# Kernel optimization log

Hardware: AMD Instinct MI355X
Metric: run time of the kernel (lower is better)

Reference implementation:

```python
import jax, jax.numpy as jnp
import numpy as np
from jax import lax

B, C, H, W = 8, 256, 128, 128
RED = 16


def _disk(r):
    yy, xx = np.mgrid[-r:r + 1, -r:r + 1]
    return ((xx * xx + yy * yy) <= r * r).astype(np.float32)


def _se_conv(m, se):
    kern = jnp.asarray(se)[None, None]  # [1,1,k,k]
    return lax.conv_general_dilated(m, kern, (1, 1), 'SAME',
                                    dimension_numbers=('NCHW', 'OIHW', 'NCHW'))


def _dilate(m, se):
    return (_se_conv(m, se) > 0.5).astype(m.dtype)


def _erode(m, se):
    return (_se_conv(m, se) > float(se.sum()) - 0.5).astype(m.dtype)


def _morph(mask):
    # GPU-friendly analogue of morphologic_process (skimage CPU round-trip):
    # invert, opening(disk2) ~ remove_small_objects(20), closing(disk1) ~
    # remove_small_holes(10), pad-3 binary_closing(disk3), crop, invert.
    d1, d2, d3 = _disk(1), _disk(2), _disk(3)
    m = 1.0 - mask
    m = _dilate(_erode(m, d2), d2)
    m = _erode(_dilate(m, d1), d1)
    mp = jnp.pad(m, ((0, 0), (0, 0), (3, 3), (3, 3)))
    mp = _erode(_dilate(mp, d3), d3)
    return 1.0 - mp[:, :, 3:-3, 3:-3]


def _conv1x1(x, w, b):
    return jnp.einsum('oi,bihw->bohw', w, x) + b[None, :, None, None]


def _avg3(x):
    # torch AvgPool2d(3,1,1) with count_include_pad=True -> always /9
    return lax.reduce_window(x, 0.0, lax.add, (1, 1, 3, 3), (1, 1, 1, 1), 'SAME') / 9.0


def _max3(x):
    return lax.reduce_window(x, -jnp.inf, lax.max, (1, 1, 3, 3), (1, 1, 1, 1), 'SAME')


def setup_inputs() -> dict:
    key = jax.random.key(0)
    ks = iter(jax.random.split(key, 32))
    s = 0.05
    d = {
        'x_p': jax.random.normal(next(ks), (B, C, H, W), jnp.float32),
        'x_c': jax.random.normal(next(ks), (B, C, H, W), jnp.float32),
        # PALayer: conv_p (shared two 1x1), conv_c (2c->c)
        'pa_w1': jax.random.normal(next(ks), (C, C), jnp.float32) * s,
        'pa_b1': jnp.zeros((C,), jnp.float32),
        'pa_w2': jax.random.normal(next(ks), (C, C), jnp.float32) * s,
        'pa_b2': jnp.zeros((C,), jnp.float32),
        'pa_wc': jax.random.normal(next(ks), (C, 2 * C), jnp.float32) * s,
        'pa_bc': jnp.zeros((C,), jnp.float32),
        # CALayer: conv_avg and conv_max (c -> c/16 -> c)
        'ca_aw1': jax.random.normal(next(ks), (C // RED, C), jnp.float32) * s,
        'ca_ab1': jnp.zeros((C // RED,), jnp.float32),
        'ca_aw2': jax.random.normal(next(ks), (C, C // RED), jnp.float32) * s,
        'ca_ab2': jnp.zeros((C,), jnp.float32),
        'ca_mw1': jax.random.normal(next(ks), (C // RED, C), jnp.float32) * s,
        'ca_mb1': jnp.zeros((C // RED,), jnp.float32),
        'ca_mw2': jax.random.normal(next(ks), (C, C // RED), jnp.float32) * s,
        'ca_mb2': jnp.zeros((C,), jnp.float32),
        # b1/b2/b3 1x1 convs
        'b1_w': jax.random.normal(next(ks), (C, C), jnp.float32) * s,
        'b1_b': jnp.zeros((C,), jnp.float32),
        'b2_w': jax.random.normal(next(ks), (C, C), jnp.float32) * s,
        'b2_b': jnp.zeros((C,), jnp.float32),
        'b3_w': jax.random.normal(next(ks), (C, C), jnp.float32) * s,
        'b3_b': jnp.zeros((C,), jnp.float32),
        # fusion: (2c+1) -> c
        'fus_w': jax.random.normal(next(ks), (C, 2 * C + 1), jnp.float32) * s,
        'fus_b': jnp.zeros((C,), jnp.float32),
    }
    return d


def reference(x_p, x_c, pa_w1, pa_b1, pa_w2, pa_b2, pa_wc, pa_bc,
              ca_aw1, ca_ab1, ca_aw2, ca_ab2, ca_mw1, ca_mb1, ca_mw2, ca_mb2,
              b1_w, b1_b, b2_w, b2_b, b3_w, b3_b, fus_w, fus_b):
    b, c, h, w = x_p.shape
    # --- PALayer(x_p) ---
    y1 = _avg3(x_p)
    y2 = _max3(x_p)
    y3 = _conv1x1(jax.nn.relu(_conv1x1(y1, pa_w1, pa_b1)), pa_w2, pa_b2)
    y4 = _conv1x1(jax.nn.relu(_conv1x1(y2, pa_w1, pa_b1)), pa_w2, pa_b2)
    pa_gate = jax.nn.sigmoid(_conv1x1(jnp.concatenate([y1 + y3, y2 + y4], axis=1), pa_wc, pa_bc))
    buffer_p = pa_gate * x_p
    # --- CALayer(x_c) ---
    a = jnp.mean(x_c, axis=(2, 3), keepdims=True)
    m = jnp.max(x_c, axis=(2, 3), keepdims=True)
    ya = _conv1x1(jax.nn.relu(_conv1x1(a, ca_aw1, ca_ab1)), ca_aw2, ca_ab2)
    ym = _conv1x1(jax.nn.relu(_conv1x1(m, ca_mw1, ca_mb1)), ca_mw2, ca_mb2)
    buffer_c = jax.nn.sigmoid(ya + ym) * x_c
    # --- cross-modal width attention ---
    Q1 = _conv1x1(buffer_p, b1_w, b1_b)
    S1 = _conv1x1(buffer_c, b2_w, b2_b)
    M_c_to_p = jax.nn.softmax(jnp.einsum('bchi,bchj->bhij', Q1, S1), axis=-1)
    Q2 = _conv1x1(buffer_c, b1_w, b1_b)
    S2 = _conv1x1(buffer_p, b2_w, b2_b)
    M_p_to_c = jax.nn.softmax(jnp.einsum('bchi,bchj->bhij', Q2, S2), axis=-1)
    # validity mask (detached) + morphology
    V = (jnp.sum(lax.stop_gradient(M_p_to_c), axis=2) > 0.1).astype(x_p.dtype)  # [b,h,w]
    V = _morph(V[:, None])  # [b,1,h,w]
    # attend b3(x_c) with M_c_to_p
    v3 = _conv1x1(x_c, b3_w, b3_b)
    buf = jnp.einsum('bhij,bchj->bchi', M_c_to_p, v3)
    out = _conv1x1(jnp.concatenate([buf, x_p, V], axis=1), fus_w, fus_b)
    return out
```

## Files before the change

### kernel.cpp

```cpp
#include <hip/hip_runtime.h>
#include <hip/hip_bf16.h>
#include <math.h>

#define BB 8
#define CC 256
#define HH 128
#define WW 128
#define HWSZ (HH*WW)
#define NTOT ((size_t)BB*CC*HWSZ)

typedef __hip_bfloat16 bf16;
typedef __attribute__((ext_vector_type(8))) short short8v;
typedef __attribute__((ext_vector_type(4))) float f32x4;

__device__ __forceinline__ float ldf(const float* p) { return *p; }
__device__ __forceinline__ float ldf(const bf16* p) { return __bfloat162float(*p); }
__device__ __forceinline__ void stf(float* p, float v) { *p = v; }
__device__ __forceinline__ void stf(bf16* p, float v) { *p = __float2bfloat16(v); }

union bfu { bf16 b; unsigned short u; };
__device__ __forceinline__ unsigned short f2bf_bits(float v) { bfu c; c.b = __float2bfloat16(v); return c.u; }
__device__ __forceinline__ float bfbits2f(unsigned short u) { bfu c; c.u = u; return __bfloat162float(c.b); }
__device__ __forceinline__ unsigned pk2(float a, float b) {
    return (unsigned)f2bf_bits(a) | ((unsigned)f2bf_bits(b) << 16);
}

__device__ __forceinline__ void gld16(const void* g, void* l) {
    __builtin_amdgcn_global_load_lds(
        (const __attribute__((address_space(1))) unsigned int*)(uintptr_t)g,
        (__attribute__((address_space(3))) unsigned int*)(uintptr_t)l, 16, 0, 0);
}

__global__ __launch_bounds__(256) void pool3_kernel(const float* __restrict__ x,
                                                    bf16* __restrict__ yavg,
                                                    bf16* __restrict__ ymax) {
    size_t idx = (size_t)blockIdx.x * 256 + threadIdx.x;
    int w0 = (int)(idx & 15) * 8;
    int h = (int)(idx >> 4) & 127;
    size_t bc = idx >> 11;
    const float* base = x + bc * HWSZ;
    float ts[8], tm[8];
#pragma unroll
    for (int i = 0; i < 8; ++i) { ts[i] = 0.f; tm[i] = -INFINITY; }
#pragma unroll
    for (int dy = -1; dy <= 1; ++dy) {
        int hh = h + dy;
        if (hh < 0 || hh >= HH) continue;
        const float* rp = base + hh * WW + w0;
        float4 v0 = *(const float4*)rp;
        float4 v1 = *(const float4*)(rp + 4);
        float s9[10], m9[10];
        s9[1] = v0.x; s9[2] = v0.y; s9[3] = v0.z; s9[4] = v0.w;
        s9[5] = v1.x; s9[6] = v1.y; s9[7] = v1.z; s9[8] = v1.w;
#pragma unroll
        for (int i = 1; i < 9; ++i) m9[i] = s9[i];
        if (w0 > 0)      { float L = rp[-1]; s9[0] = L; m9[0] = L; }
        else             { s9[0] = 0.f; m9[0] = -INFINITY; }
        if (w0 < WW - 8) { float R = rp[8]; s9[9] = R; m9[9] = R; }
        else             { s9[9] = 0.f; m9[9] = -INFINITY; }
#pragma unroll
        for (int i = 0; i < 8; ++i) {
            ts[i] += s9[i] + s9[i + 1] + s9[i + 2];
            tm[i] = fmaxf(tm[i], fmaxf(m9[i], fmaxf(m9[i + 1], m9[i + 2])));
        }
    }
    uint4 ua, um;
    ua.x = pk2(ts[0] * (1.f/9.f), ts[1] * (1.f/9.f));
    ua.y = pk2(ts[2] * (1.f/9.f), ts[3] * (1.f/9.f));
    ua.z = pk2(ts[4] * (1.f/9.f), ts[5] * (1.f/9.f));
    ua.w = pk2(ts[6] * (1.f/9.f), ts[7] * (1.f/9.f));
    um.x = pk2(tm[0], tm[1]); um.y = pk2(tm[2], tm[3]);
    um.z = pk2(tm[4], tm[5]); um.w = pk2(tm[6], tm[7]);
    *(uint4*)(yavg + idx * 8) = ua;
    *(uint4*)(ymax + idx * 8) = um;
}

__global__ __launch_bounds__(256) void prep_w_kernel(
    const float* __restrict__ w0, const float* __restrict__ w1,
    const float* __restrict__ w2, const float* __restrict__ w3,
    const float* __restrict__ w4, const float* __restrict__ w5,
    const float* __restrict__ w6, short* __restrict__ dst)
{
    int gid = blockIdx.x * 256 + threadIdx.x;
    const float* src; int K, WS, local; size_t dofs;
    if (gid < 65536)       { src = w0; K = 256; WS = 256; dofs = 0;      local = gid; }
    else if (gid < 131072) { src = w1; K = 256; WS = 256; dofs = 131072; local = gid - 65536; }
    else if (gid < 262144) { src = w2; K = 512; WS = 512; dofs = 262144; local = gid - 131072; }
    else if (gid < 327680) { src = w3; K = 256; WS = 256; dofs = 524288; local = gid - 262144; }
    else if (gid < 393216) { src = w4; K = 256; WS = 256; dofs = 655360; local = gid - 327680; }
    else if (gid < 458752) { src = w5; K = 256; WS = 256; dofs = 786432; local = gid - 393216; }
    else                   { src = w6; K = 512; WS = 513; dofs = 917504; local = gid - 458752; }
    int o = (K == 256) ? (local >> 8) : (local >> 9);
    int k = local & (K - 1);
    int kt = k >> 6, k6 = k & 63, k5 = k6 & 31;
    int pos = (k6 >> 5) * 32 + ((k5 >> 2) & 3) * 8 + (k5 >> 4) * 4 + (k5 & 3);
    pos ^= (o & 7) << 3;
    size_t off = dofs + (size_t)(o >> 7) * K * 128 + (size_t)kt * 8192 + (size_t)(o & 127) * 64 + pos;
    float v = src[(size_t)o * WS + k];
    unsigned short hb = f2bf_bits(v);
    dst[off] = (short)hb;
    dst[off + (size_t)256 * K] = (short)f2bf_bits(v - bfbits2f(hb));
}

#define EPI_NONE   0
#define EPI_RELU   1
#define EPI_ADDAUX 2
#define EPI_SIGMUL 3

#define BMP 128
#define BNO 128

template<bool SC, class T>
__device__ __forceinline__ unsigned short ld_bits(const T* p, float s);
template<> __device__ __forceinline__ unsigned short ld_bits<false, bf16>(const bf16* p, float) {
    bfu c; c.b = *p; return c.u;
}
template<> __device__ __forceinline__ unsigned short ld_bits<true, bf16>(const bf16* p, float s) {
    return f2bf_bits(__bfloat162float(*p) * s);
}
template<> __device__ __forceinline__ unsigned short ld_bits<false, float>(const float* p, float) {
    return f2bf_bits(*p);
}
template<> __device__ __forceinline__ unsigned short ld_bits<true, float>(const float* p, float s) {
    return f2bf_bits(*p * s);
}

template<bool SC, class T>
__device__ __forceinline__ void stage_X(short* __restrict__ Xs,
                                        const T* __restrict__ in,
                                        const float* __restrict__ scale,
                                        int b, int cbase, size_t pbase, int tid)
{
    const int xp  = tid & 127;
    const int xkh = (tid >> 7) * 32;
    const T* src = in + ((size_t)b * 256 + cbase + xkh) * HWSZ + pbase + xp;
    const float* scp = SC ? (scale + b * 256 + cbase + xkh) : nullptr;
    const int swz = (xp & 7) << 3;
    short* dst = Xs + xp * 64;
#pragma unroll
    for (int g = 0; g < 4; ++g) {
        unsigned short u[8];
#pragma unroll
        for (int j = 0; j < 8; ++j) {
            int k5 = (j >> 2) * 16 + g * 4 + (j & 3);
            u[j] = ld_bits<SC, T>(src + (size_t)k5 * HWSZ, SC ? scp[k5] : 1.f);
        }
        uint4 wv;
        wv.x = (unsigned)u[0] | ((unsigned)u[1] << 16);
        wv.y = (unsigned)u[2] | ((unsigned)u[3] << 16);
        wv.z = (unsigned)u[4] | ((unsigned)u[5] << 16);
        wv.w = (unsigned)u[6] | ((unsigned)u[7] << 16);
        *(uint4*)(dst + ((xkh + g * 8) ^ swz)) = wv;
    }
}

__device__ __forceinline__ void stage_rm(short* __restrict__ Xs, const bf16* __restrict__ src,
                                         size_t rstride, int k0, int tid)
{
    const int row = tid & 127;
    const int kh = (tid >> 7) * 32;
    const short* sp = (const short*)src + (size_t)row * rstride + k0 + kh;
    const int swz = (row & 7) << 3;
    short* dst = Xs + row * 64;
    short8v lv[4];
#pragma unroll
    for (int q = 0; q < 4; ++q) lv[q] = *(const short8v*)(sp + q * 8);
#pragma unroll
    for (int g = 0; g < 4; ++g) {
        unsigned short u[8];
#pragma unroll
        for (int r = 0; r < 4; ++r) {
            u[r]     = (unsigned short)lv[g >> 1][(g & 1) * 4 + r];
            u[4 + r] = (unsigned short)lv[2 + (g >> 1)][(g & 1) * 4 + r];
        }
        uint4 wv;
        wv.x = (unsigned)u[0] | ((unsigned)u[1] << 16);
        wv.y = (unsigned)u[2] | ((unsigned)u[3] << 16);
        wv.z = (unsigned)u[4] | ((unsigned)u[5] << 16);
        wv.w = (unsigned)u[6] | ((unsigned)u[7] << 16);
        *(uint4*)(dst + ((kh + g * 8) ^ swz)) = wv;
    }
}

__device__ __forceinline__ void load4f(const bf16* p, float* v) {
    ushort4 u = *(const ushort4*)p;
    v[0] = bfbits2f(u.x); v[1] = bfbits2f(u.y); v[2] = bfbits2f(u.z); v[3] = bfbits2f(u.w);
}
__device__ __forceinline__ void load4f(const float* p, float* v) {
    float4 u = *(const float4*)p;
    v[0] = u.x; v[1] = u.y; v[2] = u.z; v[3] = u.w;
}
__device__ __forceinline__ void store4(bf16* p, const float* v) {
    uint2 u;
    u.x = pk2(v[0], v[1]);
    u.y = pk2(v[2], v[3]);
    *(uint2*)p = u;
}
__device__ __forceinline__ void store4(float* p, const float* v) {
    *(float4*)p = make_float4(v[0], v[1], v[2], v[3]);
}

template<int MODE, bool TWO_IN, bool HAS_SCALE, bool HAS_V,
         class TIN1, class TIN2, class TAUX, class TOUT>
__global__ __launch_bounds__(256) void conv1x1_kernel(
    TOUT* __restrict__ out,
    const TIN1* __restrict__ in1,
    const TIN2* __restrict__ in2,
    const short* __restrict__ Wp,
    const float* __restrict__ bias,
    const TAUX* __restrict__ aux,
    const float* __restrict__ scale,
    const float* __restrict__ vvec,
    const float* __restrict__ vw, int vws)
{
    const int K = TWO_IN ? 512 : 256;
    __shared__ __align__(16) short Xs[BMP * 64];
    __shared__ __align__(16) short Wh[BNO * 64];
    __shared__ __align__(16) short Wl[BNO * 64];
    const int tid = threadIdx.x;
    const int b = blockIdx.z;
    const size_t p0 = (size_t)blockIdx.x * BMP;
    const int o0 = blockIdx.y * BNO;
    const int lane = tid & 63;
    const int wave = tid >> 6;
    const int wr = wave >> 1, wc = wave & 1;
    const int lrow = lane & 15, lg = lane >> 4;
    const int sA = (lrow & 7) << 3;

    f32x4 acc[4][4];
#pragma unroll
    for (int mi = 0; mi < 4; ++mi)
#pragma unroll
        for (int ni = 0; ni < 4; ++ni) acc[mi][ni] = (f32x4)(0.f);

    for (int kt = 0; kt < K / 64; ++kt) {
        const int k0 = kt * 64;
        {
            const short* gWh = Wp + (size_t)(o0 >> 7) * K * 128 + (size_t)kt * 8192;
            const short* gWl = gWh + (size_t)256 * K;
            const int wofs = wave * 4096;
            const int lb = lane * 16;
#pragma unroll
            for (int q = 0; q < 4; ++q) {
                gld16((const char*)gWh + wofs + q * 1024 + lb, (char*)Wh + wofs + q * 1024);
                gld16((const char*)gWl + wofs + q * 1024 + lb, (char*)Wl + wofs + q * 1024);
            }
        }
        if (TWO_IN && k0 >= 256)
            stage_X<false, TIN2>(Xs, in2, nullptr, b, k0 - 256, p0, tid);
        else
            stage_X<HAS_SCALE, TIN1>(Xs, in1, scale, b, k0, p0, tid);
        __syncthreads();
#pragma unroll
        for (int kk = 0; kk < 2; ++kk) {
            const int kofs = kk * 32 + lg * 8;
            short8v af[4], bh[4], bl[4];
#pragma unroll
            for (int mi = 0; mi < 4; ++mi)
                af[mi] = *(const short8v*)&Xs[(wr * 64 + mi * 16 + lrow) * 64 + (kofs ^ sA)];
#pragma unroll
            for (int ni = 0; ni < 4; ++ni) {
                bh[ni] = *(const short8v*)&Wh[(wc * 64 + ni * 16 + lrow) * 64 + (kofs ^ sA)];
                bl[ni] = *(const short8v*)&Wl[(wc * 64 + ni * 16 + lrow) * 64 + (kofs ^ sA)];
            }
#pragma unroll
            for (int mi = 0; mi < 4; ++mi)
#pragma unroll
                for (int ni = 0; ni < 4; ++ni)
                    acc[mi][ni] = __builtin_amdgcn_mfma_f32_16x16x32_bf16(af[mi], bh[ni], acc[mi][ni], 0, 0, 0);
#pragma unroll
            for (int mi = 0; mi < 4; ++mi)
#pragma unroll
                for (int ni = 0; ni < 4; ++ni)
                    acc[mi][ni] = __builtin_amdgcn_mfma_f32_16x16x32_bf16(af[mi], bl[ni], acc[mi][ni], 0, 0, 0);
        }
        __syncthreads();
    }

#pragma unroll
    for (int ni = 0; ni < 4; ++ni) {
        const int o = o0 + wc * 64 + ni * 16 + lrow;
        const float bs = bias[o];
        const float vwo = HAS_V ? vw[(size_t)o * vws] : 0.f;
#pragma unroll
        for (int mi = 0; mi < 4; ++mi) {
            const size_t p = p0 + wr * 64 + mi * 16 + lg * 4;
            const size_t oidx = ((size_t)b * CC + o) * HWSZ + p;
            float auxv[4];
            if (MODE == EPI_ADDAUX || MODE == EPI_SIGMUL) load4f(&aux[oidx], auxv);
            float vv[4];
            if (HAS_V) load4f(&vvec[(size_t)b * HWSZ + p], vv);
            float vals[4];
#pragma unroll
            for (int r = 0; r < 4; ++r) {
                float val = acc[mi][ni][r] + bs;
                if (HAS_V) val += vwo * vv[r];
                if (MODE == EPI_RELU)        val = fmaxf(val, 0.f);
                else if (MODE == EPI_ADDAUX) val += auxv[r];
                else if (MODE == EPI_SIGMUL) val = (1.f / (1.f + __expf(-val))) * auxv[r];
                vals[r] = val;
            }
            store4(&out[oidx], vals);
        }
    }
}

__global__ __launch_bounds__(256) void ca_reduce_kernel(const float* __restrict__ xc,
                                                        float* __restrict__ avgv,
                                                        float* __restrict__ maxv) {
    int bc = blockIdx.x;
    const float4* base = (const float4*)(xc + (size_t)bc * HWSZ);
    float s = 0.f, mx = -INFINITY;
    for (int i = threadIdx.x; i < HWSZ / 4; i += 256) {
        float4 v = base[i];
        s += v.x + v.y + v.z + v.w;
        mx = fmaxf(mx, fmaxf(fmaxf(v.x, v.y), fmaxf(v.z, v.w)));
    }
    for (int off = 32; off; off >>= 1) {
        s += __shfl_down(s, off);
        mx = fmaxf(mx, __shfl_down(mx, off));
    }
    __shared__ float ss[4], sm[4];
// ... 27 lines not shown
        ha[t] = fmaxf(s, 0.f);
    } else if (t < 32) {
        int r = t - 16;
        float s = mb1[r];
        for (int i = 0; i < 256; ++i) s += mw1[r * 256 + i] * mv[i];
        hm[r] = fmaxf(s, 0.f);
    }
    __syncthreads();
    float ya = ab2[t], ym = mb2[t];
    for (int r = 0; r < 16; ++r) {
        ya += aw2[t * 16 + r] * ha[r];
        ym += mw2[t * 16 + r] * hm[r];
    }
    float g = ya + ym;
    gate[b * 256 + t] = 1.f / (1.f + __expf(-g));
}

template<bool STORE_M>
__global__ __launch_bounds__(256) void attn_kernel(
    const bf16* __restrict__ Q, const bf16* __restrict__ S,
    bf16* __restrict__ Mout, float* __restrict__ m0out)
{
    int bh = blockIdx.x; int b = bh >> 7, h = bh & 127;
    const bf16* Qb = Q + (size_t)b * CC * HWSZ + h * WW;
    const bf16* Sb = S + (size_t)b * CC * HWSZ + h * WW;
    __shared__ __align__(16) short Qs[128 * 64];
    __shared__ __align__(16) short Ss[128 * 64];
    const int tid = threadIdx.x;
    const int lane = tid & 63, wave = tid >> 6;
    const int lrow = lane & 15, lg = lane >> 4;
    const int sA = (lrow & 7) << 3;

    f32x4 acc[2][8];
#pragma unroll
    for (int mi = 0; mi < 2; ++mi)
#pragma unroll
        for (int ni = 0; ni < 8; ++ni) acc[mi][ni] = (f32x4)(0.f);

    for (int kt = 0; kt < 4; ++kt) {
        const int k0 = kt * 64;
        {
            const int xp = tid & 127, xkh = (tid >> 7) * 32;
            const bf16* sq = Qb + (size_t)(k0 + xkh) * HWSZ + xp;
            const bf16* ssrc = Sb + (size_t)(k0 + xkh) * HWSZ + xp;
            const int swz = (xp & 7) << 3;
            short* dq = Qs + xp * 64;
            short* dsx = Ss + xp * 64;
#pragma unroll
            for (int g = 0; g < 4; ++g) {
                unsigned short uq[8], us[8];
#pragma unroll
                for (int j = 0; j < 8; ++j) {
                    int k5 = (j >> 2) * 16 + g * 4 + (j & 3);
                    bfu cq; cq.b = sq[(size_t)k5 * HWSZ]; uq[j] = cq.u;
                    bfu cs2; cs2.b = ssrc[(size_t)k5 * HWSZ]; us[j] = cs2.u;
                }
                uint4 a, s2;
                a.x = (unsigned)uq[0] | ((unsigned)uq[1] << 16);
                a.y = (unsigned)uq[2] | ((unsigned)uq[3] << 16);
                a.z = (unsigned)uq[4] | ((unsigned)uq[5] << 16);
                a.w = (unsigned)uq[6] | ((unsigned)uq[7] << 16);
                s2.x = (unsigned)us[0] | ((unsigned)us[1] << 16);
                s2.y = (unsigned)us[2] | ((unsigned)us[3] << 16);
                s2.z = (unsigned)us[4] | ((unsigned)us[5] << 16);
                s2.w = (unsigned)us[6] | ((unsigned)us[7] << 16);
                *(uint4*)(dq + ((xkh + g * 8) ^ swz)) = a;
                *(uint4*)(dsx + ((xkh + g * 8) ^ swz)) = s2;
            }
        }
        __syncthreads();
#pragma unroll
        for (int kk = 0; kk < 2; ++kk) {
            const int kofs = (kk * 32 + lg * 8) ^ sA;
            short8v qa[2], sv[8];
#pragma unroll
            for (int mi = 0; mi < 2; ++mi)
                qa[mi] = *(const short8v*)&Qs[(wave * 32 + mi * 16 + lrow) * 64 + kofs];
#pragma unroll
            for (int ni = 0; ni < 8; ++ni)
                sv[ni] = *(const short8v*)&Ss[(ni * 16 + lrow) * 64 + kofs];
#pragma unroll
            for (int mi = 0; mi < 2; ++mi)
#pragma unroll
                for (int ni = 0; ni < 8; ++ni)
                    acc[mi][ni] = __builtin_amdgcn_mfma_f32_16x16x32_bf16(qa[mi], sv[ni], acc[mi][ni], 0, 0, 0);
        }
        __syncthreads();
    }

#pragma unroll
    for (int mi = 0; mi < 2; ++mi) {
#pragma unroll
        for (int r = 0; r < 4; ++r) {
            float mx = acc[mi][0][r];
#pragma unroll
            for (int ni = 1; ni < 8; ++ni) mx = fmaxf(mx, acc[mi][ni][r]);
            for (int m = 1; m < 16; m <<= 1) mx = fmaxf(mx, __shfl_xor(mx, m));
            float sm = 0.f;
#pragma unroll
            for (int ni = 0; ni < 8; ++ni) {
                float e = __expf(acc[mi][ni][r] - mx);
                acc[mi][ni][r] = e; sm += e;
            }
            for (int m = 1; m < 16; m <<= 1) sm += __shfl_xor(sm, m);
            float inv = 1.f / sm;
#pragma unroll
            for (int ni = 0; ni < 8; ++ni) acc[mi][ni][r] *= inv;
        }
    }

    if (STORE_M) {
        bf16* Mb = Mout + (size_t)bh * WW * WW;
#pragma unroll
        for (int mi = 0; mi < 2; ++mi)
#pragma unroll
            for (int r = 0; r < 4; ++r) {
                int i = wave * 32 + mi * 16 + lg * 4 + r;
#pragma unroll
                for (int ni = 0; ni < 8; ++ni)
                    stf(&Mb[i * WW + ni * 16 + lrow], acc[mi][ni][r]);
            }
    } else {
        __shared__ float cs[16][128];
#pragma unroll
        for (int ni = 0; ni < 8; ++ni) {
            float s = 0.f;
#pragma unroll
            for (int mi = 0; mi < 2; ++mi)
#pragma unroll
                for (int r = 0; r < 4; ++r) s += acc[mi][ni][r];
            cs[wave * 4 + lg][ni * 16 + lrow] = s;
        }
        __syncthreads();
        if (tid < 128) {
            float s = 0.f;
#pragma unroll
            for (int g = 0; g < 16; ++g) s += cs[g][tid];
            m0out[(size_t)b * HWSZ + h * WW + tid] = (s > 0.1f) ? 0.f : 1.f;
        }
    }
}

__global__ __launch_bounds__(256) void attn_apply_kernel(
    const bf16* __restrict__ Mbuf, const bf16* __restrict__ v3,
    bf16* __restrict__ outb)
{
    int bh = blockIdx.x; int b = bh >> 7, h = bh & 127;
    int ch0 = blockIdx.y * 128;
    const bf16* Mb = Mbuf + (size_t)bh * WW * WW;
    const bf16* Vb = v3 + ((size_t)b * CC + ch0) * HWSZ + h * WW;
    bf16* Ob = outb + ((size_t)b * CC + ch0) * HWSZ + h * WW;
    __shared__ __align__(16) short Ms[128 * 64];
    __shared__ __align__(16) short Vs[128 * 64];
    const int tid = threadIdx.x;
    const int lane = tid & 63, wave = tid >> 6;
    const int lrow = lane & 15, lg = lane >> 4;
    const int sA = (lrow & 7) << 3;

    f32x4 acc[2][8];
#pragma unroll
    for (int mi = 0; mi < 2; ++mi)
#pragma unroll
        for (int ni = 0; ni < 8; ++ni) acc[mi][ni] = (f32x4)(0.f);

    for (int kt = 0; kt < 2; ++kt) {
        const int k0 = kt * 64;
        stage_rm(Ms, Mb, WW, k0, tid);
        stage_rm(Vs, Vb, HWSZ, k0, tid);
        __syncthreads();
#pragma unroll
        for (int kk = 0; kk < 2; ++kk) {
            const int kofs = (kk * 32 + lg * 8) ^ sA;
            short8v ma[2], vv[8];
#pragma unroll
            for (int mi = 0; mi < 2; ++mi)
                ma[mi] = *(const short8v*)&Ms[(wave * 32 + mi * 16 + lrow) * 64 + kofs];
#pragma unroll
            for (int ni = 0; ni < 8; ++ni)
                vv[ni] = *(const short8v*)&Vs[(ni * 16 + lrow) * 64 + kofs];
#pragma unroll
            for (int mi = 0; mi < 2; ++mi)
#pragma unroll
                for (int ni = 0; ni < 8; ++ni)
                    acc[mi][ni] = __builtin_amdgcn_mfma_f32_16x16x32_bf16(ma[mi], vv[ni], acc[mi][ni], 0, 0, 0);
        }
        __syncthreads();
    }

#pragma unroll
    for (int ni = 0; ni < 8; ++ni) {
// ... 73 lines not shown
    const float* fus_b = (const float*)d_in[23];
    float* out = (float*)d_out;

    char* wsb = (char*)d_ws;
    bf16* A  = (bf16*)wsb;
    bf16* Bb = (bf16*)(wsb + NTOT * 2);
    float* smalls = (float*)(wsb + NTOT * 4);
    float* avgv = smalls;
    float* maxv = smalls + 2048;
    float* gate = smalls + 4096;
    float* mph0 = smalls + 6144;
    float* mph1 = mph0 + 143648;
    float* Vfin = mph1 + 143648;
    short* Wprep = (short*)(wsb + NTOT * 4 + 1703936);
    const short* Wp_paw1 = Wprep + 0;
    const short* Wp_paw2 = Wprep + 131072;
    const short* Wp_pawc = Wprep + 262144;
    const short* Wp_b1   = Wprep + 524288;
    const short* Wp_b2   = Wprep + 655360;
    const short* Wp_b3   = Wprep + 786432;
    const short* Wp_fus  = Wprep + 917504;
    bf16* D1 = (bf16*)d_out;
    bf16* D2 = D1 + NTOT;
    bf16* Mbuf = D1;

    dim3 cgrid(HWSZ / BMP, CC / BNO, BB);
    const int TPB = 256;

    prep_w_kernel<<<2304, TPB, 0, stream>>>(pa_w1, pa_w2, pa_wc, b1_w, b2_w, b3_w, fus_w, Wprep);

    pool3_kernel<<<NTOT / 8 / 256, TPB, 0, stream>>>(x_p, A, Bb);
    conv1x1_kernel<EPI_RELU, false, false, false, bf16, bf16, bf16, bf16>
        <<<cgrid, TPB, 0, stream>>>(D1, A, nullptr, Wp_paw1, pa_b1,
                                    nullptr, nullptr, nullptr, nullptr, 0);
    conv1x1_kernel<EPI_ADDAUX, false, false, false, bf16, bf16, bf16, bf16>
        <<<cgrid, TPB, 0, stream>>>(D2, D1, nullptr, Wp_paw2, pa_b2,
                                    A, nullptr, nullptr, nullptr, 0);
    conv1x1_kernel<EPI_RELU, false, false, false, bf16, bf16, bf16, bf16>
        <<<cgrid, TPB, 0, stream>>>(A, Bb, nullptr, Wp_paw1, pa_b1,
                                    nullptr, nullptr, nullptr, nullptr, 0);
    conv1x1_kernel<EPI_ADDAUX, false, false, false, bf16, bf16, bf16, bf16>
        <<<cgrid, TPB, 0, stream>>>(D1, A, nullptr, Wp_paw2, pa_b2,
                                    Bb, nullptr, nullptr, nullptr, 0);
    conv1x1_kernel<EPI_SIGMUL, true, false, false, bf16, bf16, float, bf16>
        <<<cgrid, TPB, 0, stream>>>(A, D2, D1, Wp_pawc, pa_bc,
                                    x_p, nullptr, nullptr, nullptr, 0);

    ca_reduce_kernel<<<BB * CC, TPB, 0, stream>>>(x_c, avgv, maxv);
    ca_mlp_kernel<<<BB, TPB, 0, stream>>>(avgv, maxv, ca_aw1, ca_ab1, ca_aw2, ca_ab2,
                                          ca_mw1, ca_mb1, ca_mw2, ca_mb2, gate);

    conv1x1_kernel<EPI_NONE, false, false, false, bf16, bf16, bf16, bf16>
        <<<cgrid, TPB, 0, stream>>>(Bb, A, nullptr, Wp_b1, b1_b,
                                    nullptr, nullptr, nullptr, nullptr, 0);
    conv1x1_kernel<EPI_NONE, false, false, false, bf16, bf16, bf16, bf16>
        <<<cgrid, TPB, 0, stream>>>(D1, A, nullptr, Wp_b2, b2_b,
                                    nullptr, nullptr, nullptr, nullptr, 0);
    conv1x1_kernel<EPI_NONE, false, true, false, float, float, float, bf16>
        <<<cgrid, TPB, 0, stream>>>(A, x_c, nullptr, Wp_b1, b1_b,
                                    nullptr, gate, nullptr, nullptr, 0);
    conv1x1_kernel<EPI_NONE, false, true, false, float, float, float, bf16>
        <<<cgrid, TPB, 0, stream>>>(D2, x_c, nullptr, Wp_b2, b2_b,
                                    nullptr, gate, nullptr, nullptr, 0);

    attn_kernel<false><<<BB * HH, TPB, 0, stream>>>(A, D1, nullptr, mph0);
    attn_kernel<true><<<BB * HH, TPB, 0, stream>>>(Bb, D2, Mbuf, nullptr);

    conv1x1_kernel<EPI_NONE, false, false, false, float, float, float, bf16>
        <<<cgrid, TPB, 0, stream>>>(A, x_c, nullptr, Wp_b3, b3_b,
                                    nullptr, nullptr, nullptr, nullptr, 0);

    morph_kernel<<<512, TPB, 0, stream>>>(mph0, mph1, 128, 128, 2, 12.5f);
    morph_kernel<<<512, TPB, 0, stream>>>(mph1, mph0, 128, 128, 2, 0.5f);
    morph_kernel<<<512, TPB, 0, stream>>>(mph0, mph1, 128, 128, 1, 0.5f);
    morph_kernel<<<512, TPB, 0, stream>>>(mph1, mph0, 128, 128, 1, 4.5f);
    pad3_kernel<<<562, TPB, 0, stream>>>(mph0, mph1);
    morph_kernel<<<562, TPB, 0, stream>>>(mph1, mph0, 134, 134, 3, 0.5f);
    morph_kernel<<<562, TPB, 0, stream>>>(mph0, mph1, 134, 134, 3, 28.5f);
    vfinal_kernel<<<512, TPB, 0, stream>>>(mph1, Vfin);

    attn_apply_kernel<<<dim3(BB * HH, 2), TPB, 0, stream>>>(Mbuf, A, Bb);
    conv1x1_kernel<EPI_NONE, true, false, true, bf16, float, float, float>
        <<<cgrid, TPB, 0, stream>>>(out, Bb, x_p, Wp_fus, fus_b,
                                    nullptr, nullptr, Vfin, fus_w + 512, 513);
}
```

Measured before the change: 1.414 ms.

## Switch intermediates to pixel-major pre-swizzled bf16 layout with direct LDS loads

Intermediate activations now use a pixel-major layout whose channels are pre-permuted and XOR-swizzled to match the MFMA fragment order. This lets the new conv_mf_kernel and the attention kernels stage tiles straight into LDS with global_load_lds instead of doing strided per-element gathers and repacking. The pooling kernel and a new gated x_c prep kernel transpose through shared memory to write this layout. The gated x_c is also converted to bf16 once and reused by both projections. The cost is extra transpose kernels, and the b3 and fusion convs still read the old channel-major layout.

```diff
diff --git a/kernel.cpp b/kernel.cpp
--- a/kernel.cpp
+++ b/kernel.cpp
@@ -31,14 +31,24 @@
         (__attribute__((address_space(3))) unsigned int*)(uintptr_t)l, 16, 0, 0);
 }
 
-__global__ __launch_bounds__(256) void pool3_kernel(const float* __restrict__ x,
-                                                    bf16* __restrict__ yavg,
-                                                    bf16* __restrict__ ymax) {
-    size_t idx = (size_t)blockIdx.x * 256 + threadIdx.x;
-    int w0 = (int)(idx & 15) * 8;
-    int h = (int)(idx >> 4) & 127;
-    size_t bc = idx >> 11;
-    const float* base = x + bc * HWSZ;
+__device__ __forceinline__ int mf_p64(int c) {
+    return ((c >> 5) & 1) * 32 + ((c >> 2) & 3) * 8 + ((c >> 4) & 1) * 4 + (c & 3);
+}
+
+__global__ __launch_bounds__(256) void pool3_mf_kernel(const float* __restrict__ x,
+                                                       bf16* __restrict__ yavg,
+                                                       bf16* __restrict__ ymax) {
+    int bi = blockIdx.x;
+    int pxb = bi & 63;
+    int cb  = (bi >> 6) & 31;
+    int b   = bi >> 11;
+    int tid = threadIdx.x;
+    int cl  = tid >> 5;
+    int pxl = (tid & 31) * 8;
+    int c   = cb * 8 + cl;
+    int px  = pxb * 256 + pxl;
+    int h   = px >> 7, w0 = px & 127;
+    const float* base = x + ((size_t)b * 256 + c) * HWSZ;
     float ts[8], tm[8];
 #pragma unroll
     for (int i = 0; i < 8; ++i) { ts[i] = 0.f; tm[i] = -INFINITY; }
@@ -64,15 +74,79 @@
             tm[i] = fmaxf(tm[i], fmaxf(m9[i], fmaxf(m9[i + 1], m9[i + 2])));
         }
     }
-    uint4 ua, um;
-    ua.x = pk2(ts[0] * (1.f/9.f), ts[1] * (1.f/9.f));
-    ua.y = pk2(ts[2] * (1.f/9.f), ts[3] * (1.f/9.f));
-    ua.z = pk2(ts[4] * (1.f/9.f), ts[5] * (1.f/9.f));
-    ua.w = pk2(ts[6] * (1.f/9.f), ts[7] * (1.f/9.f));
-    um.x = pk2(tm[0], tm[1]); um.y = pk2(tm[2], tm[3]);
-    um.z = pk2(tm[4], tm[5]); um.w = pk2(tm[6], tm[7]);
-    *(uint4*)(yavg + idx * 8) = ua;
-    *(uint4*)(ymax + idx * 8) = um;
+    __shared__ short La[8][256];
+    __shared__ short Lm[8][256];
+    {
+        uint4 ua, um;
+        ua.x = pk2(ts[0]*(1.f/9.f), ts[1]*(1.f/9.f));
+        ua.y = pk2(ts[2]*(1.f/9.f), ts[3]*(1.f/9.f));
+        ua.z = pk2(ts[4]*(1.f/9.f), ts[5]*(1.f/9.f));
+        ua.w = pk2(ts[6]*(1.f/9.f), ts[7]*(1.f/9.f));
+        um.x = pk2(tm[0], tm[1]); um.y = pk2(tm[2], tm[3]);
+        um.z = pk2(tm[4], tm[5]); um.w = pk2(tm[6], tm[7]);
+        *(uint4*)&La[cl][pxl] = ua;
+        *(uint4*)&Lm[cl][pxl] = um;
+    }
+    __syncthreads();
+    int pg = pxb * 256 + tid;
+    unsigned short a8[8], m8[8];
+#pragma unroll
+    for (int i = 0; i < 8; ++i) { a8[i] = (unsigned short)La[i][tid]; m8[i] = (unsigned short)Lm[i][tid]; }
+    size_t rowb = ((size_t)b * 16384 + pg) * 256;
+    int swz = (pg & 7) << 3;
+    int c0 = cb * 8;
+#pragma unroll
+    for (int q = 0; q < 2; ++q) {
+        int cc = c0 + q * 4;
+        int col = (cc >> 6) * 64 + (mf_p64(cc & 63) ^ swz);
+        uint2 ua, um;
+        ua.x = (unsigned)a8[q*4+0] | ((unsigned)a8[q*4+1] << 16);
+        ua.y = (unsigned)a8[q*4+2] | ((unsigned)a8[q*4+3] << 16);
+        um.x = (unsigned)m8[q*4+0] | ((unsigned)m8[q*4+1] << 16);
+        um.y = (unsigned)m8[q*4+2] | ((unsigned)m8[q*4+3] << 16);
+        *(uint2*)((short*)yavg + rowb + col) = ua;
+        *(uint2*)((short*)ymax + rowb + col) = um;
+    }
+}
+
+__global__ __launch_bounds__(256) void xcs_prep_kernel(const float* __restrict__ xc,
+                                                       const float* __restrict__ gate,
+                                                       bf16* __restrict__ dst) {
+    int bi = blockIdx.x;
+    int pxb = bi & 63;
+    int cb  = (bi >> 6) & 31;
+    int b   = bi >> 11;
+    int tid = threadIdx.x;
+    int cl  = tid >> 5;
+    int pxl = (tid & 31) * 8;
+    int c   = cb * 8 + cl;
+    int px  = pxb * 256 + pxl;
+    const float* rp = xc + ((size_t)b * 256 + c) * HWSZ + px;
+    float g = gate[b * 256 + c];
+    float4 v0 = *(const float4*)rp;
+    float4 v1 = *(const float4*)(rp + 4);
+    __shared__ short L[8][256];
+    uint4 u;
+    u.x = pk2(v0.x * g, v0.y * g); u.y = pk2(v0.z * g, v0.w * g);
+    u.z = pk2(v1.x * g, v1.y * g); u.w = pk2(v1.z * g, v1.w * g);
+    *(uint4*)&L[cl][pxl] = u;
+    __syncthreads();
+    int pg = pxb * 256 + tid;
+    unsigned short a8[8];
+#pragma unroll
+    for (int i = 0; i < 8; ++i) a8[i] = (unsigned short)L[i][tid];
+    size_t rowb = ((size_t)b * 16384 + pg) * 256;
+    int swz = (pg & 7) << 3;
+    int c0 = cb * 8;
+#pragma unroll
+    for (int q = 0; q < 2; ++q) {
+        int cc = c0 + q * 4;
+        int col = (cc >> 6) * 64 + (mf_p64(cc & 63) ^ swz);
+        uint2 ua;
+        ua.x = (unsigned)a8[q*4+0] | ((unsigned)a8[q*4+1] << 16);
+        ua.y = (unsigned)a8[q*4+2] | ((unsigned)a8[q*4+3] << 16);
+        *(uint2*)((short*)dst + rowb + col) = ua;
+    }
 }
 
 __global__ __launch_bounds__(256) void prep_w_kernel(
@@ -92,9 +166,8 @@
     else                   { src = w6; K = 512; WS = 513; dofs = 917504; local = gid - 458752; }
     int o = (K == 256) ? (local >> 8) : (local >> 9);
     int k = local & (K - 1);
-    int kt = k >> 6, k6 = k & 63, k5 = k6 & 31;
-    int pos = (k6 >> 5) * 32 + ((k5 >> 2) & 3) * 8 + (k5 >> 4) * 4 + (k5 & 3);
-    pos ^= (o & 7) << 3;
+    int kt = k >> 6, k6 = k & 63;
+    int pos = mf_p64(k6) ^ ((o & 7) << 3);
     size_t off = dofs + (size_t)(o >> 7) * K * 128 + (size_t)kt * 8192 + (size_t)(o & 127) * 64 + pos;
     float v = src[(size_t)o * WS + k];
     unsigned short hb = f2bf_bits(v);
@@ -107,22 +180,137 @@
 #define EPI_ADDAUX 2
 #define EPI_SIGMUL 3
 
-#define BMP 128
-#define BNO 128
+__device__ __forceinline__ void load4f(const bf16* p, float* v) {
+    ushort4 u = *(const ushort4*)p;
+    v[0] = bfbits2f(u.x); v[1] = bfbits2f(u.y); v[2] = bfbits2f(u.z); v[3] = bfbits2f(u.w);
+}
+__device__ __forceinline__ void load4f(const float* p, float* v) {
+    float4 u = *(const float4*)p;
+    v[0] = u.x; v[1] = u.y; v[2] = u.z; v[3] = u.w;
+}
+__device__ __forceinline__ void store4(bf16* p, const float* v) {
+    uint2 u; u.x = pk2(v[0], v[1]); u.y = pk2(v[2], v[3]);
+    *(uint2*)p = u;
+}
+__device__ __forceinline__ void store4(float* p, const float* v) {
+    *(float4*)p = make_float4(v[0], v[1], v[2], v[3]);
+}
+
+template<int MODE, bool TWO_IN, class TAUX>
+__global__ __launch_bounds__(256) void conv_mf_kernel(
+    bf16* __restrict__ out,
+    const bf16* __restrict__ in1,
+    const bf16* __restrict__ in2,
+    const short* __restrict__ Wp,
+    const float* __restrict__ bias,
+    const TAUX* __restrict__ aux)
+{
+    const int K = TWO_IN ? 512 : 256;
+    __shared__ __align__(16) short Xs[128 * 64];
+    __shared__ __align__(16) short Wh[128 * 64];
+    __shared__ __align__(16) short Wl[128 * 64];
+    const int tid = threadIdx.x;
+    const int b = blockIdx.z;
+    const int p0 = blockIdx.x * 128;
+    const int o0 = blockIdx.y * 128;
+    const int lane = tid & 63, wave = tid >> 6;
+    const int wr = wave >> 1, wc = wave & 1;
+    const int lrow = lane & 15, lg = lane >> 4;
+    const int sA = (lrow & 7) << 3;
+
+    f32x4 acc[4][4];
+#pragma unroll
+    for (int mi = 0; mi < 4; ++mi)
+#pragma unroll
+        for (int ni = 0; ni < 4; ++ni) acc[mi][ni] = (f32x4)(0.f);
+
+    for (int kt = 0; kt < K / 64; ++kt) {
+        {
+            const short* gWh = Wp + (size_t)(o0 >> 7) * K * 128 + (size_t)kt * 8192;
+            const short* gWl = gWh + (size_t)256 * K;
+            const int wofs = wave * 4096;
+            const int lb = lane * 16;
+#pragma unroll
+            for (int q = 0; q < 4; ++q) {
+                gld16((const char*)gWh + wofs + q * 1024 + lb, (char*)Wh + wofs + q * 1024);
+                gld16((const char*)gWl + wofs + q * 1024 + lb, (char*)Wl + wofs + q * 1024);
+            }
+        }
+        {
+            const bf16* src = (TWO_IN && kt >= 4) ? in2 : in1;
+            const int ktl = (TWO_IN && kt >= 4) ? kt - 4 : kt;
+            const char* gX = (const char*)src + (((size_t)b * 16384 + p0) * 256 + ktl * 64) * 2;
+            const int lofs = (lane >> 3) * 512 + (lane & 7) * 16;
+#pragma unroll
+            for (int q = 0; q < 4; ++q) {
+                gld16(gX + (size_t)(wave * 32 + q * 8) * 512 + lofs,
+                      (char*)Xs + wave * 4096 + q * 1024);
+            }
+        }
+        __syncthreads();
+#pragma unroll
+        for (int kk = 0; kk < 2; ++kk) {
+            const int kofs = (kk * 32 + lg * 8) ^ sA;
+            short8v aw[4], al[4], bx[4];
+#pragma unroll
+            for (int mi = 0; mi < 4; ++mi) {
+                aw[mi] = *(const short8v*)&Wh[(wr * 64 + mi * 16 + lrow) * 64 + kofs];
+                al[mi] = *(const short8v*)&Wl[(wr * 64 + mi * 16 + lrow) * 64 + kofs];
+            }
+#pragma unroll
+            for (int ni = 0; ni < 4; ++ni)
+                bx[ni] = *(const short8v*)&Xs[(wc * 64 + ni * 16 + lrow) * 64 + kofs];
+#pragma unroll
+            for (int mi = 0; mi < 4; ++mi)
+#pragma unroll
+                for (int ni = 0; ni < 4; ++ni)
+                    acc[mi][ni] = __builtin_amdgcn_mfma_f32_16x16x32_bf16(aw[mi], bx[ni], acc[mi][ni], 0, 0, 0);
+#pragma unroll
+            for (int mi = 0; mi < 4; ++mi)
+#pragma unroll
+                for (int ni = 0; ni < 4; ++ni)
+                    acc[mi][ni] = __builtin_amdgcn_mfma_f32_16x16x32_bf16(al[mi], bx[ni], acc[mi][ni], 0, 0, 0);
+        }
+        __syncthreads();
+    }
+
+#pragma unroll
+    for (int mi = 0; mi < 4; ++mi) {
+        const int ob = o0 + wr * 64 + mi * 16 + lg * 4;
+        float b4[4];
+        load4f(&bias[ob], b4);
+        const int pcol = (ob >> 6) * 64 + mf_p64(ob & 63);
+#pragma unroll
+        for (int ni = 0; ni < 4; ++ni) {
+            const int px = p0 + wc * 64 + ni * 16 + lrow;
+            const size_t rowb = ((size_t)b * 16384 + px) * 256;
+            const size_t ad = rowb + ((size_t)pcol ^ (size_t)((px & 7) << 3));
+            float vals[4];
+            float auxv[4];
+            if (MODE == EPI_ADDAUX) load4f((const bf16*)aux + ad, auxv);
+#pragma unroll
+            for (int r = 0; r < 4; ++r) {
+                float val = acc[mi][ni][r] + b4[r];
+                if (MODE == EPI_RELU) val = fmaxf(val, 0.f);
+                else if (MODE == EPI_ADDAUX) val += auxv[r];
+                else if (MODE == EPI_SIGMUL) {
+                    float xp = ((const float*)aux)[((size_t)b * 256 + ob + r) * HWSZ + px];
+                    val = (1.f / (1.f + __expf(-val))) * xp;
+                }
+                vals[r] = val;
+            }
+            store4((bf16*)out + ad, vals);
+        }
+    }
+}
 
 template<bool SC, class T>
 __device__ __forceinline__ unsigned short ld_bits(const T* p, float s);
 template<> __device__ __forceinline__ unsigned short ld_bits<false, bf16>(const bf16* p, float) {
     bfu c; c.b = *p; return c.u;
 }
-template<> __device__ __forceinline__ unsigned short ld_bits<true, bf16>(const bf16* p, float s) {
-    return f2bf_bits(__bfloat162float(*p) * s);
-}
 template<> __device__ __forceinline__ unsigned short ld_bits<false, float>(const float* p, float) {
     return f2bf_bits(*p);
-}
-template<> __device__ __forceinline__ unsigned short ld_bits<true, float>(const float* p, float s) {
-    return f2bf_bits(*p * s);
 }
 
 template<bool SC, class T>
@@ -134,7 +322,6 @@
     const int xp  = tid & 127;
     const int xkh = (tid >> 7) * 32;
     const T* src = in + ((size_t)b * 256 + cbase + xkh) * HWSZ + pbase + xp;
-    const float* scp = SC ? (scale + b * 256 + cbase + xkh) : nullptr;
     const int swz = (xp & 7) << 3;
     short* dst = Xs + xp * 64;
 #pragma unroll
@@ -143,7 +330,7 @@
 #pragma unroll
         for (int j = 0; j < 8; ++j) {
             int k5 = (j >> 2) * 16 + g * 4 + (j & 3);
-            u[j] = ld_bits<SC, T>(src + (size_t)k5 * HWSZ, SC ? scp[k5] : 1.f);
+            u[j] = ld_bits<SC, T>(src + (size_t)k5 * HWSZ, 1.f);
         }
         uint4 wv;
         wv.x = (unsigned)u[0] | ((unsigned)u[1] << 16);
@@ -154,75 +341,25 @@
     }
 }
 
-__device__ __forceinline__ void stage_rm(short* __restrict__ Xs, const bf16* __restrict__ src,
-                                         size_t rstride, int k0, int tid)
-{
-    const int row = tid & 127;
-    const int kh = (tid >> 7) * 32;
-    const short* sp = (const short*)src + (size_t)row * rstride + k0 + kh;
-    const int swz = (row & 7) << 3;
-    short* dst = Xs + row * 64;
-    short8v lv[4];
-#pragma unroll
-    for (int q = 0; q < 4; ++q) lv[q] = *(const short8v*)(sp + q * 8);
-#pragma unroll
-    for (int g = 0; g < 4; ++g) {
-        unsigned short u[8];
-#pragma unroll
-        for (int r = 0; r < 4; ++r) {
-            u[r]     = (unsigned short)lv[g >> 1][(g & 1) * 4 + r];
-            u[4 + r] = (unsigned short)lv[2 + (g >> 1)][(g & 1) * 4 + r];
-        }
-        uint4 wv;
-        wv.x = (unsigned)u[0] | ((unsigned)u[1] << 16);
-        wv.y = (unsigned)u[2] | ((unsigned)u[3] << 16);
-        wv.z = (unsigned)u[4] | ((unsigned)u[5] << 16);
-        wv.w = (unsigned)u[6] | ((unsigned)u[7] << 16);
-        *(uint4*)(dst + ((kh + g * 8) ^ swz)) = wv;
-    }
-}
-
-__device__ __forceinline__ void load4f(const bf16* p, float* v) {
-    ushort4 u = *(const ushort4*)p;
-    v[0] = bfbits2f(u.x); v[1] = bfbits2f(u.y); v[2] = bfbits2f(u.z); v[3] = bfbits2f(u.w);
-}
-__device__ __forceinline__ void load4f(const float* p, float* v) {
-    float4 u = *(const float4*)p;
-    v[0] = u.x; v[1] = u.y; v[2] = u.z; v[3] = u.w;
-}
-__device__ __forceinline__ void store4(bf16* p, const float* v) {
-    uint2 u;
-    u.x = pk2(v[0], v[1]);
-    u.y = pk2(v[2], v[3]);
-    *(uint2*)p = u;
-}
-__device__ __forceinline__ void store4(float* p, const float* v) {
-    *(float4*)p = make_float4(v[0], v[1], v[2], v[3]);
-}
-
-template<int MODE, bool TWO_IN, bool HAS_SCALE, bool HAS_V,
-         class TIN1, class TIN2, class TAUX, class TOUT>
+template<int MODE, bool TWO_IN, bool HAS_V, class TIN1, class TIN2, class TOUT>
 __global__ __launch_bounds__(256) void conv1x1_kernel(
     TOUT* __restrict__ out,
     const TIN1* __restrict__ in1,
     const TIN2* __restrict__ in2,
     const short* __restrict__ Wp,
     const float* __restrict__ bias,
-    const TAUX* __restrict__ aux,
-    const float* __restrict__ scale,
     const float* __restrict__ vvec,
     const float* __restrict__ vw, int vws)
 {
     const int K = TWO_IN ? 512 : 256;
-    __shared__ __align__(16) short Xs[BMP * 64];
-    __shared__ __align__(16) short Wh[BNO * 64];
-    __shared__ __align__(16) short Wl[BNO * 64];
+    __shared__ __align__(16) short Xs[128 * 64];
+    __shared__ __align__(16) short Wh[128 * 64];
+    __shared__ __align__(16) short Wl[128 * 64];
     const int tid = threadIdx.x;
     const int b = blockIdx.z;
-    const size_t p0 = (size_t)blockIdx.x * BMP;
-    const int o0 = blockIdx.y * BNO;
-    const int lane = tid & 63;
-    const int wave = tid >> 6;
+    const size_t p0 = (size_t)blockIdx.x * 128;
+    const int o0 = blockIdx.y * 128;
+    const int lane = tid & 63, wave = tid >> 6;
     const int wr = wave >> 1, wc = wave & 1;
     const int lrow = lane & 15, lg = lane >> 4;
     const int sA = (lrow & 7) << 3;
@@ -249,19 +386,19 @@
         if (TWO_IN && k0 >= 256)
             stage_X<false, TIN2>(Xs, in2, nullptr, b, k0 - 256, p0, tid);
         else
-            stage_X<HAS_SCALE, TIN1>(Xs, in1, scale, b, k0, p0, tid);
+            stage_X<false, TIN1>(Xs, in1, nullptr, b, k0, p0, tid);
         __syncthreads();
 #pragma unroll
         for (int kk = 0; kk < 2; ++kk) {
-            const int kofs = kk * 32 + lg * 8;
+            const int kofs = (kk * 32 + lg * 8) ^ sA;
             short8v af[4], bh[4], bl[4];
 #pragma unroll
             for (int mi = 0; mi < 4; ++mi)
-                af[mi] = *(const short8v*)&Xs[(wr * 64 + mi * 16 + lrow) * 64 + (kofs ^ sA)];
+                af[mi] = *(const short8v*)&Xs[(wr * 64 + mi * 16 + lrow) * 64 + kofs];
 #pragma unroll
             for (int ni = 0; ni < 4; ++ni) {
-                bh[ni] = *(const short8v*)&Wh[(wc * 64 + ni * 16 + lrow) * 64 + (kofs ^ sA)];
-                bl[ni] = *(const short8v*)&Wl[(wc * 64 + ni * 16 + lrow) * 64 + (kofs ^ sA)];
+                bh[ni] = *(const short8v*)&Wh[(wc * 64 + ni * 16 + lrow) * 64 + kofs];
+                bl[ni] = *(const short8v*)&Wl[(wc * 64 + ni * 16 + lrow) * 64 + kofs];
             }
 #pragma unroll
             for (int mi = 0; mi < 4; ++mi)
@@ -286,8 +423,6 @@
         for (int mi = 0; mi < 4; ++mi) {
             const size_t p = p0 + wr * 64 + mi * 16 + lg * 4;
             const size_t oidx = ((size_t)b * CC + o) * HWSZ + p;
-            float auxv[4];
-            if (MODE == EPI_ADDAUX || MODE == EPI_SIGMUL) load4f(&aux[oidx], auxv);
             float vv[4];
             if (HAS_V) load4f(&vvec[(size_t)b * HWSZ + p], vv);
             float vals[4];
@@ -295,9 +430,6 @@
             for (int r = 0; r < 4; ++r) {
                 float val = acc[mi][ni][r] + bs;
                 if (HAS_V) val += vwo * vv[r];
-                if (MODE == EPI_RELU)        val = fmaxf(val, 0.f);
-                else if (MODE == EPI_ADDAUX) val += auxv[r];
-                else if (MODE == EPI_SIGMUL) val = (1.f / (1.f + __expf(-val))) * auxv[r];
                 vals[r] = val;
             }
             store4(&out[oidx], vals);
@@ -371,8 +503,8 @@
     bf16* __restrict__ Mout, float* __restrict__ m0out)
 {
     int bh = blockIdx.x; int b = bh >> 7, h = bh & 127;
-    const bf16* Qb = Q + (size_t)b * CC * HWSZ + h * WW;
-    const bf16* Sb = S + (size_t)b * CC * HWSZ + h * WW;
+    const char* Qb = (const char*)Q + ((size_t)(b * 16384 + h * 128)) * 512;
+    const char* Sb = (const char*)S + ((size_t)(b * 16384 + h * 128)) * 512;
     __shared__ __align__(16) short Qs[128 * 64];
     __shared__ __align__(16) short Ss[128 * 64];
     const int tid = threadIdx.x;
@@ -387,35 +519,11 @@
         for (int ni = 0; ni < 8; ++ni) acc[mi][ni] = (f32x4)(0.f);
 
     for (int kt = 0; kt < 4; ++kt) {
-        const int k0 = kt * 64;
-        {
-            const int xp = tid & 127, xkh = (tid >> 7) * 32;
-            const bf16* sq = Qb + (size_t)(k0 + xkh) * HWSZ + xp;
-            const bf16* ssrc = Sb + (size_t)(k0 + xkh) * HWSZ + xp;
-            const int swz = (xp & 7) << 3;
-            short* dq = Qs + xp * 64;
-            short* dsx = Ss + xp * 64;
-#pragma unroll
-            for (int g = 0; g < 4; ++g) {
-                unsigned short uq[8], us[8];
-#pragma unroll
-                for (int j = 0; j < 8; ++j) {
-                    int k5 = (j >> 2) * 16 + g * 4 + (j & 3);
-                    bfu cq; cq.b = sq[(size_t)k5 * HWSZ]; uq[j] = cq.u;
-                    bfu cs2; cs2.b = ssrc[(size_t)k5 * HWSZ]; us[j] = cs2.u;
-                }
-                uint4 a, s2;
-                a.x = (unsigned)uq[0] | ((unsigned)uq[1] << 16);
-                a.y = (unsigned)uq[2] | ((unsigned)uq[3] << 16);
-                a.z = (unsigned)uq[4] | ((unsigned)uq[5] << 16);
-                a.w = (unsigned)uq[6] | ((unsigned)uq[7] << 16);
-                s2.x = (unsigned)us[0] | ((unsigned)us[1] << 16);
-                s2.y = (unsigned)us[2] | ((unsigned)us[3] << 16);
-                s2.z = (unsigned)us[4] | ((unsigned)us[5] << 16);
-                s2.w = (unsigned)us[6] | ((unsigned)us[7] << 16);
-                *(uint4*)(dq + ((xkh + g * 8) ^ swz)) = a;
-                *(uint4*)(dsx + ((xkh + g * 8) ^ swz)) = s2;
-            }
+        const int lofs = (lane >> 3) * 512 + (lane & 7) * 16 + kt * 128;
+#pragma unroll
+        for (int q = 0; q < 4; ++q) {
+            gld16(Qb + (size_t)(wave * 32 + q * 8) * 512 + lofs, (char*)Qs + wave * 4096 + q * 1024);
+            gld16(Sb + (size_t)(wave * 32 + q * 8) * 512 + lofs, (char*)Ss + wave * 4096 + q * 1024);
         }
         __syncthreads();
 #pragma unroll
@@ -459,16 +567,19 @@
     }
 
     if (STORE_M) {
-        bf16* Mb = Mout + (size_t)bh * WW * WW;
-#pragma unroll
-        for (int mi = 0; mi < 2; ++mi)
-#pragma unroll
-            for (int r = 0; r < 4; ++r) {
-                int i = wave * 32 + mi * 16 + lg * 4 + r;
-#pragma unroll
-                for (int ni = 0; ni < 8; ++ni)
-                    stf(&Mb[i * WW + ni * 16 + lrow], acc[mi][ni][r]);
-            }
+        short* Mb = (short*)Mout + (size_t)bh * 16384;
+#pragma unroll
+        for (int ni = 0; ni < 8; ++ni) {
+            int j = ni * 16 + lrow;
+            int pj = (j >> 6) * 64 + mf_p64(j & 63);
+#pragma unroll
+            for (int mi = 0; mi < 2; ++mi)
+#pragma unroll
+                for (int r = 0; r < 4; ++r) {
+                    int i = wave * 32 + mi * 16 + lg * 4 + r;
+                    Mb[i * 128 + (pj ^ ((i & 7) << 3))] = (short)f2bf_bits(acc[mi][ni][r]);
+                }
+        }
     } else {
         __shared__ float cs[16][128];
 #pragma unroll
@@ -487,6 +598,34 @@
             for (int g = 0; g < 16; ++g) s += cs[g][tid];
             m0out[(size_t)b * HWSZ + h * WW + tid] = (s > 0.1f) ? 0.f : 1.f;
         }
+    }
+}
+
+__device__ __forceinline__ void stage_rm(short* __restrict__ Xs, const bf16* __restrict__ src,
+                                         size_t rstride, int k0, int tid)
+{
+    const int row = tid & 127;
+    const int kh = (tid >> 7) * 32;
+    const short* sp = (const short*)src + (size_t)row * rstride + k0 + kh;
+    const int swz = (row & 7) << 3;
+    short* dst = Xs + row * 64;
+    short8v lv[4];
+#pragma unroll
+    for (int q = 0; q < 4; ++q) lv[q] = *(const short8v*)(sp + q * 8);
+#pragma unroll
+    for (int g = 0; g < 4; ++g) {
+        unsigned short u[8];
+#pragma unroll
+        for (int r = 0; r < 4; ++r) {
+            u[r]     = (unsigned short)lv[g >> 1][(g & 1) * 4 + r];
+            u[4 + r] = (unsigned short)lv[2 + (g >> 1)][(g & 1) * 4 + r];
+        }
+        uint4 wv;
+        wv.x = (unsigned)u[0] | ((unsigned)u[1] << 16);
+        wv.y = (unsigned)u[2] | ((unsigned)u[3] << 16);
+        wv.z = (unsigned)u[4] | ((unsigned)u[5] << 16);
+        wv.w = (unsigned)u[6] | ((unsigned)u[7] << 16);
+        *(uint4*)(dst + ((kh + g * 8) ^ swz)) = wv;
     }
 }
 
@@ -496,7 +635,7 @@
 {
     int bh = blockIdx.x; int b = bh >> 7, h = bh & 127;
     int ch0 = blockIdx.y * 128;
-    const bf16* Mb = Mbuf + (size_t)bh * WW * WW;
+    const char* Mb = (const char*)Mbuf + (size_t)bh * 32768;
     const bf16* Vb = v3 + ((size_t)b * CC + ch0) * HWSZ + h * WW;
     bf16* Ob = outb + ((size_t)b * CC + ch0) * HWSZ + h * WW;
     __shared__ __align__(16) short Ms[128 * 64];
@@ -514,7 +653,12 @@
 
     for (int kt = 0; kt < 2; ++kt) {
         const int k0 = kt * 64;
-        stage_rm(Ms, Mb, WW, k0, tid);
+        {
+            const int lofs = (lane >> 3) * 256 + (lane & 7) * 16 + kt * 128;
+#pragma unroll
+            for (int q = 0; q < 4; ++q)
+                gld16(Mb + (size_t)(wave * 32 + q * 8) * 256 + lofs, (char*)Ms + wave * 4096 + q * 1024);
+        }
         stage_rm(Vs, Vb, HWSZ, k0, tid);
         __syncthreads();
 #pragma unroll
@@ -634,53 +778,46 @@
     const short* Wp_fus  = Wprep + 917504;
     bf16* D1 = (bf16*)d_out;
     bf16* D2 = D1 + NTOT;
-    bf16* Mbuf = D1;
-
-    dim3 cgrid(HWSZ / BMP, CC / BNO, BB);
+    bf16* Mbuf = A;
+
+    dim3 cgrid(HWSZ / 128, 2, BB);
     const int TPB = 256;
 
     prep_w_kernel<<<2304, TPB, 0, stream>>>(pa_w1, pa_w2, pa_wc, b1_w, b2_w, b3_w, fus_w, Wprep);
-
-    pool3_kernel<<<NTOT / 8 / 256, TPB, 0, stream>>>(x_p, A, Bb);
-    conv1x1_kernel<EPI_RELU, false, false, false, bf16, bf16, bf16, bf16>
-        <<<cgrid, TPB, 0, stream>>>(D1, A, nullptr, Wp_paw1, pa_b1,
-                                    nullptr, nullptr, nullptr, nullptr, 0);
-    conv1x1_kernel<EPI_ADDAUX, false, false, false, bf16, bf16, bf16, bf16>
-        <<<cgrid, TPB, 0, stream>>>(D2, D1, nullptr, Wp_paw2, pa_b2,
-                                    A, nullptr, nullptr, nullptr, 0);
-    conv1x1_kernel<EPI_RELU, false, false, false, bf16, bf16, bf16, bf16>
-        <<<cgrid, TPB, 0, stream>>>(A, Bb, nullptr, Wp_paw1, pa_b1,
-                                    nullptr, nullptr, nullptr, nullptr, 0);
-    conv1x1_kernel<EPI_ADDAUX, false, false, false, bf16, bf16, bf16, bf16>
-        <<<cgrid, TPB, 0, stream>>>(D1, A, nullptr, Wp_paw2, pa_b2,
-                                    Bb, nullptr, nullptr, nullptr, 0);
-    conv1x1_kernel<EPI_SIGMUL, true, false, false, bf16, bf16, float, bf16>
-        <<<cgrid, TPB, 0, stream>>>(A, D2, D1, Wp_pawc, pa_bc,
-                                    x_p, nullptr, nullptr, nullptr, 0);
-
     ca_reduce_kernel<<<BB * CC, TPB, 0, stream>>>(x_c, avgv, maxv);
     ca_mlp_kernel<<<BB, TPB, 0, stream>>>(avgv, maxv, ca_aw1, ca_ab1, ca_aw2, ca_ab2,
                                           ca_mw1, ca_mb1, ca_mw2, ca_mb2, gate);
 
-    conv1x1_kernel<EPI_NONE, false, false, false, bf16, bf16, bf16, bf16>
-        <<<cgrid, TPB, 0, stream>>>(Bb, A, nullptr, Wp_b1, b1_b,
-                                    nullptr, nullptr, nullptr, nullptr, 0);
-    conv1x1_kernel<EPI_NONE, false, false, false, bf16, bf16, bf16, bf16>
-        <<<cgrid, TPB, 0, stream>>>(D1, A, nullptr, Wp_b2, b2_b,
-                                    nullptr, nullptr, nullptr, nullptr, 0);
-    conv1x1_kernel<EPI_NONE, false, true, false, float, float, float, bf16>
-        <<<cgrid, TPB, 0, stream>>>(A, x_c, nullptr, Wp_b1, b1_b,
-                                    nullptr, gate, nullptr, nullptr, 0);
-    conv1x1_kernel<EPI_NONE, false, true, false, float, float, float, bf16>
-        <<<cgrid, TPB, 0, stream>>>(D2, x_c, nullptr, Wp_b2, b2_b,
-                                    nullptr, gate, nullptr, nullptr, 0);
+    pool3_mf_kernel<<<16384, TPB, 0, stream>>>(x_p, A, Bb);
+    conv_mf_kernel<EPI_RELU, false, bf16>
+        <<<cgrid, TPB, 0, stream>>>(D1, A, nullptr, Wp_paw1, pa_b1, nullptr);
+    conv_mf_kernel<EPI_ADDAUX, false, bf16>
+        <<<cgrid, TPB, 0, stream>>>(D2, D1, nullptr, Wp_paw2, pa_b2, A);
+    conv_mf_kernel<EPI_RELU, false, bf16>
+        <<<cgrid, TPB, 0, stream>>>(A, Bb, nullptr, Wp_paw1, pa_b1, nullptr);
+    conv_mf_kernel<EPI_ADDAUX, false, bf16>
+        <<<cgrid, TPB, 0, stream>>>(D1, A, nullptr, Wp_paw2, pa_b2, Bb);
+    conv_mf_kernel<EPI_SIGMUL, true, float>
+        <<<cgrid, TPB, 0, stream>>>(A, D2, D1, Wp_pawc, pa_bc, x_p);
+
+    conv_mf_kernel<EPI_NONE, false, bf16>
+        <<<cgrid, TPB, 0, stream>>>(Bb, A, nullptr, Wp_b1, b1_b, nullptr);
+    conv_mf_kernel<EPI_NONE, false, bf16>
+        <<<cgrid, TPB, 0, stream>>>(D1, A, nullptr, Wp_b2, b2_b, nullptr);
+    xcs_prep_kernel<<<16384, TPB, 0, stream>>>(x_c, gate, D2);
+    conv_mf_kernel<EPI_NONE, false, bf16>
+        <<<cgrid, TPB, 0, stream>>>(A, D2, nullptr, Wp_b1, b1_b, nullptr);
 
     attn_kernel<false><<<BB * HH, TPB, 0, stream>>>(A, D1, nullptr, mph0);
-    attn_kernel<true><<<BB * HH, TPB, 0, stream>>>(Bb, D2, Mbuf, nullptr);
-
-    conv1x1_kernel<EPI_NONE, false, false, false, float, float, float, bf16>
-        <<<cgrid, TPB, 0, stream>>>(A, x_c, nullptr, Wp_b3, b3_b,
-                                    nullptr, nullptr, nullptr, nullptr, 0);
+
+    conv_mf_kernel<EPI_NONE, false, bf16>
+        <<<cgrid, TPB, 0, stream>>>(D1, D2, nullptr, Wp_b2, b2_b, nullptr);
+
+    attn_kernel<true><<<BB * HH, TPB, 0, stream>>>(Bb, D1, Mbuf, nullptr);
+
+    conv1x1_kernel<EPI_NONE, false, false, float, float, bf16>
+        <<<cgrid, TPB, 0, stream>>>(D2, x_c, nullptr, Wp_b3, b3_b,
+                                    nullptr, nullptr, 0);
 
     morph_kernel<<<512, TPB, 0, stream>>>(mph0, mph1, 128, 128, 2, 12.5f);
     morph_kernel<<<512, TPB, 0, stream>>>(mph1, mph0, 128, 128, 2, 0.5f);
@@ -691,8 +828,8 @@
     morph_kernel<<<562, TPB, 0, stream>>>(mph0, mph1, 134, 134, 3, 28.5f);
     vfinal_kernel<<<512, TPB, 0, stream>>>(mph1, Vfin);
 
-    attn_apply_kernel<<<dim3(BB * HH, 2), TPB, 0, stream>>>(Mbuf, A, Bb);
-    conv1x1_kernel<EPI_NONE, true, false, true, bf16, float, float, float>
+    attn_apply_kernel<<<dim3(BB * HH, 2), TPB, 0, stream>>>(Mbuf, D2, Bb);
+    conv1x1_kernel<EPI_NONE, true, true, bf16, float, float>
         <<<cgrid, TPB, 0, stream>>>(out, Bb, x_p, Wp_fus, fus_b,
-                                    nullptr, nullptr, Vfin, fus_w + 512, 513);
-}
+                                    Vfin, fus_w + 512, 513);
+}
```

After: 1.404 ms. No clear change (-0.7%).
